# Performance work log

Hardware: AMD Instinct MI355X
Metric: run time of the kernel (lower is better)

Reference implementation:

```python
import jax, jax.numpy as jnp
import numpy as np
import math

T = 4096
HID = 2048
H = 16
D = 128
RD = 64            # rotary_dim = head_dim * partial_rotary_factor (0.5)
THETA = 10000.0
EPS = 1e-6
GROUPS = 8
LAYER_IDX = 2
N_LAYERS = 32


def build_slope_tensor(num_heads):
    def get_slopes_power_of_2(n):
        start = 2 ** (-(2 ** (-(math.log2(n) - 3))))
        ratio = start
        return [start * ratio ** i for i in range(n)]
    if math.log2(num_heads).is_integer():
        return get_slopes_power_of_2(num_heads)
    closest = 2 ** math.floor(math.log2(num_heads))
    return (get_slopes_power_of_2(closest)
            + build_slope_tensor(2 * closest)[0::2][: num_heads - closest])


def compute_slope():
    base = np.array(build_slope_tensor(H), dtype=np.float32)
    return jnp.asarray(-base * (1 - (LAYER_IDX - 1) / (N_LAYERS - 1) + 1e-5), dtype=jnp.float32)


def setup_inputs() -> dict:
    key = jax.random.key(0)
    ks = jax.random.split(key, 8)
    s = 0.02
    return {
        "positions": jnp.arange(T, dtype=jnp.int32),
        "hidden_states": jax.random.normal(ks[0], (T, HID), dtype=jnp.float32),
        "recurrent_state": jnp.zeros((1, H, D, D), dtype=jnp.float32),
        "w_qkv": jax.random.normal(ks[1], (HID, 3 * H * D), dtype=jnp.float32) * s,
        "w_g": jax.random.normal(ks[2], (HID, H * D), dtype=jnp.float32) * s,
        "w_dense": jax.random.normal(ks[3], (H * D, HID), dtype=jnp.float32) * s,
        "q_norm_w": jnp.ones((D,), dtype=jnp.float32),
        "k_norm_w": jnp.ones((D,), dtype=jnp.float32),
        "g_norm_w": jnp.ones((H * D,), dtype=jnp.float32),
    }


def _rms(x, w):
    var = jnp.mean(jnp.square(x), axis=-1, keepdims=True)
    return x * jax.lax.rsqrt(var + EPS) * w


def _rope(x, positions):
    # partial neox-style rotary on first RD dims of each head
    inv_freq = 1.0 / (THETA ** (jnp.arange(0, RD, 2, dtype=jnp.float32) / RD))
    freqs = positions.astype(jnp.float32)[:, None] * inv_freq   # [T, RD/2]
    cos = jnp.cos(freqs)[:, None, :]                            # [T, 1, RD/2]
    sin = jnp.sin(freqs)[:, None, :]
    x1 = x[..., : RD // 2]
    x2 = x[..., RD // 2 : RD]
    x_pass = x[..., RD:]
    return jnp.concatenate([x1 * cos - x2 * sin, x2 * cos + x1 * sin, x_pass], axis=-1)


def reference(positions, hidden_states, recurrent_state,
              w_qkv, w_g, w_dense, q_norm_w, k_norm_w, g_norm_w):
    t = hidden_states.shape[0]
    qkv = (hidden_states @ w_qkv).reshape(t, 3, H, D)
    q, k, v = qkv[:, 0], qkv[:, 1], qkv[:, 2]
    q = _rms(q, q_norm_w)
    k = _rms(k, k_norm_w)
    q = _rope(q, positions)
    k = _rope(k, positions)

    slope = compute_slope()                    # [H], negative
    decay = jnp.exp(slope)                     # per-head per-step decay
    scale = D ** -0.5
    q = (q * scale).astype(jnp.float32)
    k = k.astype(jnp.float32)
    v = v.astype(jnp.float32)

    def step(S, qkv_t):
        q_t, k_t, v_t = qkv_t                  # each [H, D]
        S = S * decay[:, None, None] + k_t[:, :, None] * v_t[:, None, :]
        o_t = jnp.einsum('hk,hkv->hv', q_t, S)
        return S, o_t

    S0 = recurrent_state[0].astype(jnp.float32)   # [H, K, V]
    S_final, o = jax.lax.scan(step, S0, (q, k, v))
    attn = o.reshape(t, H * D)

    gate = jax.nn.sigmoid(hidden_states @ w_g)
    # GroupRMSNorm: normalize per group of size (H*D)/GROUPS, scale by full weight
    g = attn.reshape(t, GROUPS, (H * D) // GROUPS)
    var = jnp.mean(jnp.square(g), axis=-1, keepdims=True)
    g = (g * jax.lax.rsqrt(var + EPS)).reshape(t, H * D) * g_norm_w

    out = (g * gate) @ w_dense
    return out, S_final[None]
```

## Files before the change

### kernel.cpp

```cpp
#include <hip/hip_runtime.h>
#include <hip/hip_bf16.h>

using bf16x8 = __attribute__((ext_vector_type(8))) __bf16;
using f32x4  = __attribute__((ext_vector_type(4))) float;

constexpr int T_SEQ = 4096;
constexpr int HID_C = 2048;
constexpr int NH    = 16;
constexpr int QKV_N = 6144;

__device__ __forceinline__ float head_slope(int h) {
    return -exp2f(-0.5f * (float)(h + 1)) * 0.967751935483871f;
}

__device__ __forceinline__ ushort f2bfu(float f) {
    __hip_bfloat16 h = __float2bfloat16(f);
    return *(ushort*)&h;
}
__device__ __forceinline__ float bfu2f(ushort u) {
    union { unsigned int i; float f; } x; x.i = ((unsigned int)u) << 16; return x.f;
}

__device__ __forceinline__ void async16(const ushort* g, ushort* l) {
    __builtin_amdgcn_global_load_lds((const __attribute__((address_space(1))) void*)g,
                                     (__attribute__((address_space(3))) void*)l, 16, 0, 0);
}

template<int N> __device__ __forceinline__ void waitcnt_vm() {
    if constexpr (N == 0)      asm volatile("s_waitcnt vmcnt(0)" ::: "memory");
    else if constexpr (N == 2) asm volatile("s_waitcnt vmcnt(2)" ::: "memory");
    else if constexpr (N == 4) asm volatile("s_waitcnt vmcnt(4)" ::: "memory");
    else if constexpr (N == 6) asm volatile("s_waitcnt vmcnt(6)" ::: "memory");
}

__global__ __launch_bounds__(256) void cvt_bf16(const float* __restrict__ src,
                                                ushort* __restrict__ dst, int n) {
    int i = (blockIdx.x * 256 + threadIdx.x) * 8;
    if (i >= n) return;
    float4 a = *(const float4*)(src + i);
    float4 b = *(const float4*)(src + i + 4);
    ushort4 ua = {f2bfu(a.x), f2bfu(a.y), f2bfu(a.z), f2bfu(a.w)};
    ushort4 ub = {f2bfu(b.x), f2bfu(b.y), f2bfu(b.z), f2bfu(b.w)};
    *(ushort4*)(dst + i) = ua;
    *(ushort4*)(dst + i + 4) = ub;
}

__global__ __launch_bounds__(256) void transpose_cvt(const float* __restrict__ src,
                                                     ushort* __restrict__ dst,
                                                     int R, int C) {
    __shared__ ushort tile[64][68];
    int t = threadIdx.x;
    int tr = blockIdx.y * 64, tc = blockIdx.x * 64;
    int r0 = t >> 4;
    int c4 = (t & 15) << 2;
#pragma unroll
    for (int p = 0; p < 4; ++p) {
        int row = r0 + p * 16;
        float4 v = *(const float4*)&src[(size_t)(tr + row) * C + tc + c4];
        tile[row][c4 + 0] = f2bfu(v.x);
        tile[row][c4 + 1] = f2bfu(v.y);
        tile[row][c4 + 2] = f2bfu(v.z);
        tile[row][c4 + 3] = f2bfu(v.w);
    }
    __syncthreads();
#pragma unroll
    for (int p = 0; p < 4; ++p) {
        int orow = r0 + p * 16;
        ushort4 u;
        u.x = tile[c4 + 0][orow];
        u.y = tile[c4 + 1][orow];
        u.z = tile[c4 + 2][orow];
        u.w = tile[c4 + 3][orow];
        *(ushort4*)&dst[(size_t)(tc + orow) * R + tr + c4] = u;
    }
}

template<int MI, int BN>
__device__ __forceinline__ void gemm8_core(const ushort* __restrict__ Ag,
                                           const ushort* __restrict__ Bg,
                                           int K, int bm, int bn,
                                           ushort* sh, f32x4 (&acc)[MI][4]) {
    constexpr int WM = 16 / MI;
    constexpr int WN = 8 / WM;
    constexpr int SB = BN / 128;
    constexpr int AH = (MI >= 8) ? 2 : 1;
    constexpr int MH = MI / AH;

    const int tid  = threadIdx.x;
    const int lane = tid & 63;
    const int wave = tid >> 6;
    const int lane15 = lane & 15, quad = lane >> 4;
    const int wm = wave / WN, wn = wave % WN;
    const int swz = lane15 & 7;

    ushort* const ldsA0 = sh;
    ushort* const ldsA1 = sh + 16384;
    ushort* const ldsB0 = sh + 32768;
    ushort* const ldsB1 = sh + 32768 + BN * 64;

    const int srow = lane >> 3;
    const int scol = ((lane & 7) ^ srow) << 3;
    const ushort* gA = Ag + (size_t)(bm + srow) * K + scol;
    const ushort* gB = Bg + (size_t)(bn + srow) * K + scol;
    const int ro  = wave * 16;
    const int roB = wave * 8 * SB;
    const int NT = K >> 6;

#define STAGE_A(L, k0) do { \
    _Pragma("unroll") for (int h = 0; h < 2; ++h) \
    _Pragma("unroll") for (int q = 0; q < 2; ++q) \
        async16(gA + (size_t)((h) * 128 + ro + q * 8) * K + (k0), (L) + ((h) * 128 + ro + q * 8) * 64); } while (0)
#define STAGE_B(L, k0) do { \
    _Pragma("unroll") for (int h = 0; h < 2; ++h) \
    _Pragma("unroll") for (int q = 0; q < SB; ++q) \
        async16(gB + (size_t)((h) * (BN / 2) + roB + q * 8) * K + (k0), (L) + ((h) * (BN / 2) + roB + q * 8) * 64); } while (0)

    STAGE_A(ldsA0, 0);
    STAGE_B(ldsB0, 0);
    waitcnt_vm<0>();
    asm volatile("s_barrier" ::: "memory");

    for (int t = 0; t < NT; ++t) {
        const ushort* LA = (t & 1) ? ldsA1 : ldsA0;
        const ushort* LB = (t & 1) ? ldsB1 : ldsB0;
        ushort* LAn = (t & 1) ? ldsA0 : ldsA1;
        ushort* LBn = (t & 1) ? ldsB0 : ldsB1;
        bf16x8 bfr[4][2];
#pragma unroll
        for (int j = 0; j < 4; ++j)
#pragma unroll
            for (int ks = 0; ks < 2; ++ks)
                bfr[j][ks] = *(const bf16x8*)&LB[(wn * 64 + j * 16 + lane15) * 64 + (((ks * 4 + quad) ^ swz) << 3)];
        bf16x8 af0[MH][2];
#pragma unroll
        for (int i = 0; i < MH; ++i)
#pragma unroll
            for (int ks = 0; ks < 2; ++ks)
                af0[i][ks] = *(const bf16x8*)&LA[(wm * (MI * 16) + i * 16 + lane15) * 64 + (((ks * 4 + quad) ^ swz) << 3)];
        if (t + 1 < NT) {
            STAGE_A(LAn, (t + 1) << 6);
            STAGE_B(LBn, (t + 1) << 6);
        }
        __builtin_amdgcn_s_setprio(1);
#pragma unroll
        for (int i = 0; i < MH; ++i)
#pragma unroll
            for (int j = 0; j < 4; ++j)
#pragma unroll
                for (int ks = 0; ks < 2; ++ks)
                    acc[i][j] = __builtin_amdgcn_mfma_f32_16x16x32_bf16(af0[i][ks], bfr[j][ks], acc[i][j], 0, 0, 0);
        __builtin_amdgcn_s_setprio(0);
        if constexpr (AH == 2) {
            bf16x8 af1[MH][2];
#pragma unroll
            for (int i = 0; i < MH; ++i)
#pragma unroll
                for (int ks = 0; ks < 2; ++ks)
                    af1[i][ks] = *(const bf16x8*)&LA[(wm * (MI * 16) + (MH + i) * 16 + lane15) * 64 + (((ks * 4 + quad) ^ swz) << 3)];
            __builtin_amdgcn_s_setprio(1);
#pragma unroll
            for (int i = 0; i < MH; ++i)
#pragma unroll
                for (int j = 0; j < 4; ++j)
#pragma unroll
                    for (int ks = 0; ks < 2; ++ks)
                        acc[MH + i][j] = __builtin_amdgcn_mfma_f32_16x16x32_bf16(af1[i][ks], bfr[j][ks], acc[MH + i][j], 0, 0, 0);
            __builtin_amdgcn_s_setprio(0);
        }
        waitcnt_vm<0>();
        asm volatile("s_barrier" ::: "memory");
    }
#undef STAGE_A
#undef STAGE_B
}

__global__ __launch_bounds__(512, 2) void gemm_fused(const ushort* __restrict__ A,
                                                     const ushort* __restrict__ Bcat,
                                                     ushort* __restrict__ qkv,
                                                     ushort* __restrict__ gate, int K) {
    __shared__ ushort sh[65536];
    int bid = blockIdx.x;
    int x = bid & 7, w = bid >> 3;
    int rm = x >> 2, rn = x & 3;
    int wm_i = w >> 3, wn_i = w & 7;
    int bm = (rm * 8 + wm_i) * 256;
    int bn = (rn * 8 + wn_i) * 256;
    f32x4 acc[8][4] = {};
    gemm8_core<8, 256>(A, Bcat, K, bm, bn, sh, acc);

    int lane = threadIdx.x & 63, wave = threadIdx.x >> 6;
    int lane15 = lane & 15, quad = lane >> 4;
    int wm = wave >> 2, wn = wave & 3;
    bool isg = bn >= QKV_N;
    ushort* outp = isg ? gate : qkv;
    int ncol = isg ? HID_C : QKV_N;
    int cb = (isg ? bn - QKV_N : bn) + wn * 64;
    int rb = bm + wm * 128;
#pragma unroll
    for (int i = 0; i < 8; ++i)
#pragma unroll
        for (int j = 0; j < 4; ++j) {
            int col = cb + j * 16 + lane15;
#pragma unroll
            for (int r = 0; r < 4; ++r) {
                float v = acc[i][j][r];
                if (isg) v = 1.0f / (1.0f + __expf(-v));
                outp[(size_t)(rb + i * 16 + quad * 4 + r) * ncol + col] = f2bfu(v);
            }
        }
}

__global__ __launch_bounds__(512, 2) void gemm_dense(const ushort* __restrict__ A,
                                                     const ushort* __restrict__ Bt,
                                                     float* __restrict__ Cout, int N, int K) {
    __shared__ ushort sh[49152];
    int bid = blockIdx.x;
    int x = bid & 7, w = bid >> 3;
    int rm = x >> 1, rn = x & 1;
    int wm_i = w >> 3, wn_i = w & 7;
    int bm = (rm * 4 + wm_i) * 256;
    int bn = (rn * 8 + wn_i) * 128;
    f32x4 acc[4][4] = {};
    gemm8_core<4, 128>(A, Bt, K, bm, bn, sh, acc);

    int lane = threadIdx.x & 63, wave = threadIdx.x >> 6;
    int lane15 = lane & 15, quad = lane >> 4;
    int wm = wave >> 1, wn = wave & 1;
    int cb = bn + wn * 64;
    int rb = bm + wm * 64;
#pragma unroll
    for (int i = 0; i < 4; ++i)
#pragma unroll
        for (int j = 0; j < 4; ++j) {
            int col = cb + j * 16 + lane15;
#pragma unroll
            for (int r = 0; r < 4; ++r)
                Cout[(size_t)(rb + i * 16 + quad * 4 + r) * N + col] = acc[i][j][r];
        }
}

__global__ __launch_bounds__(256) void rope_tab(const int* __restrict__ positions,
                                                float2* __restrict__ tab) {
    int i = blockIdx.x * 256 + threadIdx.x;
    int t = i >> 5, fi = i & 31;
    float inv = expf((float)fi * -0.2878231366f);
    float freq = (float)positions[t] * inv;
    float sn, cs;
    sincosf(freq, &sn, &cs);
    tab[i] = make_float2(cs, sn);
}

__global__ __launch_bounds__(256) void qk_rope_T(ushort* __restrict__ qkv,
                                                 const float2* __restrict__ tab,
                                                 const float* __restrict__ qw,
                                                 const float* __restrict__ kw,
                                                 ushort* __restrict__ kT,
                                                 ushort* __restrict__ vT) {
    __shared__ ushort tile[64][132];
    int bt = blockIdx.x;
    int kind = blockIdx.y >> 4, h = blockIdx.y & 15;
    int tid = threadIdx.x;
    int row = tid >> 2, c = tid & 3, d0 = c * 32;
    int t = bt * 64 + row;
    ushort* base = qkv + (size_t)t * QKV_N + kind * 2048 + h * 128 + d0;
    bf16x8 pk[4];
#pragma unroll
    for (int p = 0; p < 4; ++p) pk[p] = *(const bf16x8*)(base + p * 8);
    if (kind < 2) {
        float x[32];
        float ss = 0.f;
#pragma unroll
        for (int p = 0; p < 4; ++p)
#pragma unroll
            for (int i = 0; i < 8; ++i) {
                x[p * 8 + i] = (float)pk[p][i];
                ss += x[p * 8 + i] * x[p * 8 + i];
            }
        ss += __shfl_xor(ss, 1);
        ss += __shfl_xor(ss, 2);
        float rr = rsqrtf(ss * (1.0f / 128.0f) + 1e-6f);
        const float* w = (kind == 0) ? qw : kw;
#pragma unroll
        for (int i = 0; i < 32; ++i) x[i] *= rr * w[d0 + i];
#pragma unroll
        for (int i = 0; i < 32; ++i) {
            float p = __shfl_xor(x[i], 1);
            if (c < 2) {
                float2 rt = tab[t * 32 + i];
                x[i] = (c == 0) ? (x[i] * rt.x - p * rt.y) : (x[i] * rt.x + p * rt.y);
            }
        }
        float sc = (kind == 0) ? 0.08838834764831845f : 1.0f;
#pragma unroll
        for (int p = 0; p < 4; ++p)
#pragma unroll
            for (int i = 0; i < 8; ++i) pk[p][i] = (__bf16)(x[p * 8 + i] * sc);
#pragma unroll
        for (int p = 0; p < 4; ++p) *(bf16x8*)(base + p * 8) = pk[p];
    }
    if (kind >= 1) {
#pragma unroll
        for (int p = 0; p < 4; ++p) {
            ushort4* s = (ushort4*)&pk[p];
            *(ushort4*)&tile[row][d0 + p * 8]     = s[0];
            *(ushort4*)&tile[row][d0 + p * 8 + 4] = s[1];
        }
        __syncthreads();
        ushort* outT = ((kind == 1) ? kT : vT) + (size_t)(h * 128) * T_SEQ + bt * 64;
        int d = tid >> 1, half = tid & 1;
#pragma unroll
        for (int tt = 0; tt < 8; ++tt) {
            int tl = half * 32 + tt * 4;
            ushort4 u;
            u.x = tile[tl + 0][d];
            u.y = tile[tl + 1][d];
            u.z = tile[tl + 2][d];
            u.w = tile[tl + 3][d];
            *(ushort4*)&outT[(size_t)d * T_SEQ + tl] = u;
        }
    }
}

__global__ __launch_bounds__(256) void chunk_partial(const ushort* __restrict__ kT,
                                                     const ushort* __restrict__ vT,
                                                     float* __restrict__ PT) {
    int c = blockIdx.x, h = blockIdx.y;
    float slope = head_slope(h);
    float lam_inv = __expf(-slope);
    int tid = threadIdx.x, lane = tid & 63, wave = tid >> 6;
    int lane15 = lane & 15, quad = lane >> 4;
    int wv = (wave & 1) * 64, wd = (wave >> 1) * 64;
    const ushort* vbase = vT + (size_t)h * 128 * T_SEQ + c * 128;
    const ushort* kbase = kT + (size_t)h * 128 * T_SEQ + c * 128;
    f32x4 acc[4][4] = {};
#pragma unroll
    for (int j0 = 0; j0 < 128; j0 += 32) {
        float w8[8];
        w8[0] = __expf(slope * (float)(127 - (j0 + quad * 8)));
#pragma unroll
        for (int kk = 1; kk < 8; ++kk) w8[kk] = w8[kk - 1] * lam_inv;
        bf16x8 afr[4], bfr[4];
#pragma unroll
        for (int i = 0; i < 4; ++i) {
            bf16x8 v = *(const bf16x8*)&vbase[(size_t)(wv + i * 16 + lane15) * T_SEQ + j0 + quad * 8];
#pragma unroll
            for (int kk = 0; kk < 8; ++kk) afr[i][kk] = (__bf16)((float)v[kk] * w8[kk]);
        }
#pragma unroll
        for (int j = 0; j < 4; ++j)
            bfr[j] = *(const bf16x8*)&kbase[(size_t)(wd + j * 16 + lane15) * T_SEQ + j0 + quad * 8];
#pragma unroll
        for (int i = 0; i < 4; ++i)
#pragma unroll
            for (int j = 0; j < 4; ++j)
                acc[i][j] = __builtin_amdgcn_mfma_f32_16x16x32_bf16(afr[i], bfr[j], acc[i][j], 0, 0, 0);
    }
    float* out = PT + ((size_t)c * 16 + h) * 16384;
#pragma unroll
    for (int i = 0; i < 4; ++i)
#pragma unroll
        for (int j = 0; j < 4; ++j)
#pragma unroll
            for (int r = 0; r < 4; ++r)
                out[(size_t)(wv + i * 16 + quad * 4 + r) * 128 + wd + j * 16 + lane15] = acc[i][j][r];
}

__global__ __launch_bounds__(128) void scan_states(const float* __restrict__ PT,
                                                   const float* __restrict__ S0,
                                                   ushort* __restrict__ Spb,
                                                   float* __restrict__ Sfin) {
    int hv = blockIdx.x;
    int d = threadIdx.x;
    int h = hv >> 7, v = hv & 127;
    float lamC = __expf(head_slope(h) * 128.0f);
    float s = S0[(size_t)h * 16384 + d * 128 + v];
#pragma unroll
    for (int c = 0; c < 32; ++c) {
        size_t idx = ((size_t)c * 2048 + hv) * 128 + d;
        Spb[idx] = f2bfu(s);
        s = s * lamC + PT[idx];
    }
    Sfin[(size_t)h * 16384 + d * 128 + v] = s;
}

__global__ __launch_bounds__(256) void chunk_out(const ushort* __restrict__ qkv,
                                                 const ushort* __restrict__ vT,
                                                 const ushort* __restrict__ Spb,
                                                 ushort* __restrict__ o) {
    int c = blockIdx.x, h = blockIdx.y;
    float slope = head_slope(h);
    __shared__ ushort Ps[128 * 136];
    int tid = threadIdx.x, lane = tid & 63, wave = tid >> 6;
    int lane15 = lane & 15, quad = lane >> 4;
    int t0 = c * 128;
    int tt0 = wave, tt1 = 7 - wave;
    const ushort* qbase = qkv + (size_t)t0 * QKV_N + h * 128;
    const ushort* kbase = qbase + 2048;

    bf16x8 qf0[4], qf1[4];
#pragma unroll
    for (int ds = 0; ds < 4; ++ds) {
        qf0[ds] = *(const bf16x8*)&qbase[(size_t)(tt0 * 16 + lane15) * QKV_N + ds * 32 + quad * 8];
        qf1[ds] = *(const bf16x8*)&qbase[(size_t)(tt1 * 16 + lane15) * QKV_N + ds * 32 + quad * 8];
    }
    f32x4 s0a[4] = {};
    f32x4 s1a[8] = {};
#pragma unroll
    for (int st = 0; st < 8; ++st) {
        if (st <= tt1) {
            bf16x8 kf[4];
#pragma unroll
            for (int ds = 0; ds < 4; ++ds)
                kf[ds] = *(const bf16x8*)&kbase[(size_t)(st * 16 + lane15) * QKV_N + ds * 32 + quad * 8];
#pragma unroll
            for (int ds = 0; ds < 4; ++ds)
                s1a[st] = __builtin_amdgcn_mfma_f32_16x16x32_bf16(qf1[ds], kf[ds], s1a[st], 0, 0, 0);
            if (st <= tt0) {
#pragma unroll
                for (int ds = 0; ds < 4; ++ds)
                    s0a[st] = __builtin_amdgcn_mfma_f32_16x16x32_bf16(qf0[ds], kf[ds], s0a[st], 0, 0, 0);
            }
        }
    }
    int stmax0 = tt0 + ((tt0 & 1) ? 0 : 1);
    int stmax1 = tt1 + ((tt1 & 1) ? 0 : 1);
#pragma unroll
    for (int st = 0; st < 8; ++st) {
        if (st <= stmax1) {
#pragma unroll
            for (int r = 0; r < 4; ++r) {
                int t = tt1 * 16 + quad * 4 + r;
                int s = st * 16 + lane15;
                float val = 0.f;
                if (st <= tt1) val = (s <= t) ? s1a[st][r] * __expf(slope * (float)(t - s)) : 0.f;
                Ps[t * 136 + s] = f2bfu(val);
            }
        }
    }
#pragma unroll
    for (int st = 0; st < 5; ++st) {
        if (st <= stmax0) {
#pragma unroll
            for (int r = 0; r < 4; ++r) {
                int t = tt0 * 16 + quad * 4 + r;
                int s = st * 16 + lane15;
                float val = 0.f;
                if (st <= tt0) val = (s <= t) ? s0a[st][r] * __expf(slope * (float)(t - s)) : 0.f;
                Ps[t * 136 + s] = f2bfu(val);
            }
        }
    }
    __syncthreads();
    f32x4 oa0[8] = {};
    f32x4 oa1[8] = {};
    float lam0 = __expf(slope * (float)(tt0 * 16 + lane15 + 1));
    float lam1 = __expf(slope * (float)(tt1 * 16 + lane15 + 1));
    bf16x8 qs0[4], qs1[4];
#pragma unroll
    for (int ds = 0; ds < 4; ++ds)
#pragma unroll
        for (int kk = 0; kk < 8; ++kk) {
            qs0[ds][kk] = (__bf16)((float)qf0[ds][kk] * lam0);
            qs1[ds][kk] = (__bf16)((float)qf1[ds][kk] * lam1);
        }
    const ushort* spb = Spb + ((size_t)c * 2048 + h * 128) * 128;
#pragma unroll
    for (int vt = 0; vt < 8; ++vt)
#pragma unroll
        for (int ds = 0; ds < 4; ++ds) {
            bf16x8 bfrag = *(const bf16x8*)&spb[(vt * 16 + lane15) * 128 + ds * 32 + quad * 8];
            oa0[vt] = __builtin_amdgcn_mfma_f32_16x16x32_bf16(qs0[ds], bfrag, oa0[vt], 0, 0, 0);
            oa1[vt] = __builtin_amdgcn_mfma_f32_16x16x32_bf16(qs1[ds], bfrag, oa1[vt], 0, 0, 0);
        }
    const ushort* vbase = vT + (size_t)h * 128 * T_SEQ + t0;
    int ns0 = (tt0 + 2) >> 1, ns1 = (tt1 + 2) >> 1;
#pragma unroll
    for (int s32 = 0; s32 < 4; ++s32) {
        if (s32 < ns1) {
            bf16x8 af = *(const bf16x8*)&Ps[(tt1 * 16 + lane15) * 136 + s32 * 32 + quad * 8];
#pragma unroll
            for (int vt = 0; vt < 8; ++vt) {
                bf16x8 bfrag = *(const bf16x8*)&vbase[(size_t)(vt * 16 + lane15) * T_SEQ + s32 * 32 + quad * 8];
                oa1[vt] = __builtin_amdgcn_mfma_f32_16x16x32_bf16(af, bfrag, oa1[vt], 0, 0, 0);
            }
        }
    }
#pragma unroll
    for (int s32 = 0; s32 < 2; ++s32) {
        if (s32 < ns0) {
            bf16x8 af = *(const bf16x8*)&Ps[(tt0 * 16 + lane15) * 136 + s32 * 32 + quad * 8];
#pragma unroll
            for (int vt = 0; vt < 8; ++vt) {
                bf16x8 bfrag = *(const bf16x8*)&vbase[(size_t)(vt * 16 + lane15) * T_SEQ + s32 * 32 + quad * 8];
                oa0[vt] = __builtin_amdgcn_mfma_f32_16x16x32_bf16(af, bfrag, oa0[vt], 0, 0, 0);
            }
        }
    }
#pragma unroll
    for (int vt = 0; vt < 8; ++vt)
#pragma unroll
        for (int r = 0; r < 4; ++r) {
            o[(size_t)(t0 + tt0 * 16 + quad * 4 + r) * 2048 + h * 128 + vt * 16 + lane15] = f2bfu(oa0[vt][r]);
            o[(size_t)(t0 + tt1 * 16 + quad * 4 + r) * 2048 + h * 128 + vt * 16 + lane15] = f2bfu(oa1[vt][r]);
        }
}

__global__ __launch_bounds__(256) void gnorm_gate(const ushort* __restrict__ o,
                                                  const ushort* __restrict__ gate,
                                                  const float* __restrict__ gw,
                                                  ushort* __restrict__ gg) {
    int t = blockIdx.x;
    int tid = threadIdx.x;
    const ushort* op = o + (size_t)t * 2048 + tid * 8;
    bf16x8 xv = *(const bf16x8*)op;
    float x[8];
    float ss = 0.0f;
#pragma unroll
    for (int i = 0; i < 8; ++i) { x[i] = (float)xv[i]; ss += x[i] * x[i]; }
#pragma unroll
    for (int off = 16; off > 0; off >>= 1) ss += __shfl_xor(ss, off);
    float r = rsqrtf(ss * (1.0f / 256.0f) + 1e-6f);
    const ushort* gp = gate + (size_t)t * 2048;
#pragma unroll
    for (int i = 0; i < 8; ++i) {
        int j = tid * 8 + i;
        float val = x[i] * r * gw[j] * bfu2f(gp[j]);
        gg[(size_t)t * 2048 + j] = f2bfu(val);
    }
}

extern "C" void kernel_launch(void* const* d_in, const int* in_sizes, int n_in,
                              void* d_out, int out_size, void* d_ws, size_t ws_size,
                              hipStream_t stream) {
    const int* positions   = (const int*)d_in[0];
    const float* hidden    = (const float*)d_in[1];
    const float* S0        = (const float*)d_in[2];
    const float* w_qkv     = (const float*)d_in[3];
    const float* w_g       = (const float*)d_in[4];
    const float* w_dense   = (const float*)d_in[5];
    const float* qw        = (const float*)d_in[6];
    const float* kw        = (const float*)d_in[7];
    const float* gw        = (const float*)d_in[8];

    char* ws = (char*)d_ws;
    ushort* qkv     = (ushort*)ws;
    ushort* wqkv_t  = (ushort*)(ws + 50331648);
    ushort* wg_t    = (ushort*)(ws + 75497472);
    float2* ropet   = (float2*)(ws + 50331648);
    float*  PT      = (float*)(ws + 50331648);
    ushort* wd_t    = (ushort*)(ws + 83886080);
    ushort* gatebuf = (ushort*)(ws + 92274688);
    ushort* hid_b   = (ushort*)(ws + 109051904);
    ushort* Spb     = (ushort*)(ws + 109051904);
    ushort* kT      = (ushort*)(ws + 125829120);
    ushort* vT      = (ushort*)(ws + 142606336);
    ushort* gg      = (ushort*)ws;

    float* out  = (float*)d_out;
    float* Sfin = out + (size_t)T_SEQ * HID_C;
    ushort* obuf = (ushort*)d_out;

    cvt_bf16<<<T_SEQ * HID_C / (256 * 8), 256, 0, stream>>>(hidden, hid_b, T_SEQ * HID_C);
    transpose_cvt<<<dim3(QKV_N / 64, HID_C / 64), 256, 0, stream>>>(w_qkv, wqkv_t, HID_C, QKV_N);
    transpose_cvt<<<dim3(HID_C / 64, HID_C / 64), 256, 0, stream>>>(w_g, wg_t, HID_C, HID_C);
    transpose_cvt<<<dim3(HID_C / 64, HID_C / 64), 256, 0, stream>>>(w_dense, wd_t, HID_C, HID_C);

    gemm_fused<<<dim3(512), 512, 0, stream>>>(hid_b, wqkv_t, qkv, gatebuf, HID_C);

    rope_tab<<<T_SEQ * 32 / 256, 256, 0, stream>>>(positions, ropet);
    qk_rope_T<<<dim3(T_SEQ / 64, 48), 256, 0, stream>>>(qkv, ropet, qw, kw, kT, vT);

    chunk_partial<<<dim3(32, 16), 256, 0, stream>>>(kT, vT, PT);
    scan_states<<<2048, 128, 0, stream>>>(PT, S0, Spb, Sfin);
    chunk_out<<<dim3(32, 16), 256, 0, stream>>>(qkv, vT, Spb, obuf);
    gnorm_gate<<<T_SEQ, 256, 0, stream>>>(obuf, gatebuf, gw, gg);

    gemm_dense<<<dim3(256), 512, 0, stream>>>(gg, wd_t, out, HID_C, HID_C);
}
```

Measured before the change: 443.2 us.

## Merge prep kernels into one launch and retile dense GEMM to 128x128 blocks

```diff
diff --git a/kernel.cpp b/kernel.cpp
--- a/kernel.cpp
+++ b/kernel.cpp
@@ -33,10 +33,9 @@
     else if constexpr (N == 6) asm volatile("s_waitcnt vmcnt(6)" ::: "memory");
 }
 
-__global__ __launch_bounds__(256) void cvt_bf16(const float* __restrict__ src,
-                                                ushort* __restrict__ dst, int n) {
-    int i = (blockIdx.x * 256 + threadIdx.x) * 8;
-    if (i >= n) return;
+__device__ __forceinline__ void cvt_body(const float* __restrict__ src, ushort* __restrict__ dst,
+                                         int bid, int tid) {
+    int i = (bid * 256 + tid) * 8;
     float4 a = *(const float4*)(src + i);
     float4 b = *(const float4*)(src + i + 4);
     ushort4 ua = {f2bfu(a.x), f2bfu(a.y), f2bfu(a.z), f2bfu(a.w)};
@@ -45,12 +44,11 @@
     *(ushort4*)(dst + i + 4) = ub;
 }
 
-__global__ __launch_bounds__(256) void transpose_cvt(const float* __restrict__ src,
-                                                     ushort* __restrict__ dst,
-                                                     int R, int C) {
-    __shared__ ushort tile[64][68];
-    int t = threadIdx.x;
-    int tr = blockIdx.y * 64, tc = blockIdx.x * 64;
+__device__ __forceinline__ void transpose_body(const float* __restrict__ src,
+                                               ushort* __restrict__ dst,
+                                               int R, int C, int bx, int by, int t,
+                                               ushort (*tile)[68]) {
+    int tr = by * 64, tc = bx * 64;
     int r0 = t >> 4;
     int c4 = (t & 15) << 2;
 #pragma unroll
@@ -72,6 +70,40 @@
         u.z = tile[c4 + 2][orow];
         u.w = tile[c4 + 3][orow];
         *(ushort4*)&dst[(size_t)(tc + orow) * R + tr + c4] = u;
+    }
+}
+
+__global__ __launch_bounds__(256) void prep_all(const float* __restrict__ hidden,
+                                                ushort* __restrict__ hid_b,
+                                                const float* __restrict__ w_qkv,
+                                                ushort* __restrict__ wqkv_t,
+                                                const float* __restrict__ w_g,
+                                                ushort* __restrict__ wg_t,
+                                                const float* __restrict__ w_dense,
+                                                ushort* __restrict__ wd_t,
+                                                const int* __restrict__ positions,
+                                                float2* __restrict__ ropet) {
+    __shared__ ushort tile[64][68];
+    int b = blockIdx.x, t = threadIdx.x;
+    if (b < 4096) {
+        cvt_body(hidden, hid_b, b, t);
+    } else if (b < 7168) {
+        int bb = b - 4096;
+        transpose_body(w_qkv, wqkv_t, HID_C, QKV_N, bb % 96, bb / 96, t, tile);
+    } else if (b < 8192) {
+        int bb = b - 7168;
+        transpose_body(w_g, wg_t, HID_C, HID_C, bb % 32, bb / 32, t, tile);
+    } else if (b < 9216) {
+        int bb = b - 8192;
+        transpose_body(w_dense, wd_t, HID_C, HID_C, bb % 32, bb / 32, t, tile);
+    } else {
+        int i = (b - 9216) * 256 + t;
+        int tt = i >> 5, fi = i & 31;
+        float inv = expf((float)fi * -0.2878231366f);
+        float freq = (float)positions[tt] * inv;
+        float sn, cs;
+        sincosf(freq, &sn, &cs);
+        ropet[i] = make_float2(cs, sn);
     }
 }
 
@@ -172,6 +204,74 @@
     }
 #undef STAGE_A
 #undef STAGE_B
+}
+
+__device__ __forceinline__ void gemm4_core(const ushort* __restrict__ Ag,
+                                           const ushort* __restrict__ Bg,
+                                           int K, int bm, int bn,
+                                           ushort* sh, f32x4 (&acc)[4][4]) {
+    const int tid  = threadIdx.x;
+    const int lane = tid & 63;
+    const int wave = tid >> 6;
+    const int lane15 = lane & 15, quad = lane >> 4;
+    const int wm = wave >> 1, wn = wave & 1;
+    const int swz = lane15 & 7;
+
+    ushort* const ldsA0 = sh;
+    ushort* const ldsA1 = sh + 8192;
+    ushort* const ldsB0 = sh + 16384;
+    ushort* const ldsB1 = sh + 24576;
+
+    const int srow = lane >> 3;
+    const int scol = ((lane & 7) ^ srow) << 3;
+    const ushort* gA = Ag + (size_t)(bm + srow) * K + scol;
+    const ushort* gB = Bg + (size_t)(bn + srow) * K + scol;
+    const int ro = wave * 32;
+    const int NT = K >> 6;
+
+#define STG(L, g, k0) do { \
+    _Pragma("unroll") for (int q = 0; q < 4; ++q) \
+        async16((g) + (size_t)(ro + q * 8) * K + (k0), (L) + (ro + q * 8) * 64); } while (0)
+
+    STG(ldsA0, gA, 0);
+    STG(ldsB0, gB, 0);
+    waitcnt_vm<0>();
+    asm volatile("s_barrier" ::: "memory");
+
+    for (int t = 0; t < NT; ++t) {
+        const ushort* LA = (t & 1) ? ldsA1 : ldsA0;
+        const ushort* LB = (t & 1) ? ldsB1 : ldsB0;
+        ushort* LAn = (t & 1) ? ldsA0 : ldsA1;
+        ushort* LBn = (t & 1) ? ldsB0 : ldsB1;
+        bf16x8 bfr[4][2];
+#pragma unroll
+        for (int j = 0; j < 4; ++j)
+#pragma unroll
+            for (int ks = 0; ks < 2; ++ks)
+                bfr[j][ks] = *(const bf16x8*)&LB[(wn * 64 + j * 16 + lane15) * 64 + (((ks * 4 + quad) ^ swz) << 3)];
+        bf16x8 af[4][2];
+#pragma unroll
+        for (int i = 0; i < 4; ++i)
+#pragma unroll
+            for (int ks = 0; ks < 2; ++ks)
+                af[i][ks] = *(const bf16x8*)&LA[(wm * 64 + i * 16 + lane15) * 64 + (((ks * 4 + quad) ^ swz) << 3)];
+        if (t + 1 < NT) {
+            STG(LAn, gA, (t + 1) << 6);
+            STG(LBn, gB, (t + 1) << 6);
+        }
+        __builtin_amdgcn_s_setprio(1);
+#pragma unroll
+        for (int i = 0; i < 4; ++i)
+#pragma unroll
+            for (int j = 0; j < 4; ++j)
+#pragma unroll
+                for (int ks = 0; ks < 2; ++ks)
+                    acc[i][j] = __builtin_amdgcn_mfma_f32_16x16x32_bf16(af[i][ks], bfr[j][ks], acc[i][j], 0, 0, 0);
+        __builtin_amdgcn_s_setprio(0);
+        waitcnt_vm<0>();
+        asm volatile("s_barrier" ::: "memory");
+    }
+#undef STG
 }
 
 __global__ __launch_bounds__(512, 2) void gemm_fused(const ushort* __restrict__ A,
@@ -210,18 +310,18 @@
         }
 }
 
-__global__ __launch_bounds__(512, 2) void gemm_dense(const ushort* __restrict__ A,
+__global__ __launch_bounds__(256, 2) void gemm_dense(const ushort* __restrict__ A,
                                                      const ushort* __restrict__ Bt,
                                                      float* __restrict__ Cout, int N, int K) {
-    __shared__ ushort sh[49152];
+    __shared__ ushort sh[32768];
     int bid = blockIdx.x;
     int x = bid & 7, w = bid >> 3;
     int rm = x >> 1, rn = x & 1;
     int wm_i = w >> 3, wn_i = w & 7;
-    int bm = (rm * 4 + wm_i) * 256;
+    int bm = (rm * 8 + wm_i) * 128;
     int bn = (rn * 8 + wn_i) * 128;
     f32x4 acc[4][4] = {};
-    gemm8_core<4, 128>(A, Bt, K, bm, bn, sh, acc);
+    gemm4_core(A, Bt, K, bm, bn, sh, acc);
 
     int lane = threadIdx.x & 63, wave = threadIdx.x >> 6;
     int lane15 = lane & 15, quad = lane >> 4;
@@ -237,17 +337,6 @@
             for (int r = 0; r < 4; ++r)
                 Cout[(size_t)(rb + i * 16 + quad * 4 + r) * N + col] = acc[i][j][r];
         }
-}
-
-__global__ __launch_bounds__(256) void rope_tab(const int* __restrict__ positions,
-                                                float2* __restrict__ tab) {
-    int i = blockIdx.x * 256 + threadIdx.x;
-    int t = i >> 5, fi = i & 31;
-    float inv = expf((float)fi * -0.2878231366f);
-    float freq = (float)positions[t] * inv;
-    float sn, cs;
-    sincosf(freq, &sn, &cs);
-    tab[i] = make_float2(cs, sn);
 }
 
 __global__ __launch_bounds__(256) void qk_rope_T(ushort* __restrict__ qkv,
@@ -546,7 +635,7 @@
     ushort* qkv     = (ushort*)ws;
     ushort* wqkv_t  = (ushort*)(ws + 50331648);
     ushort* wg_t    = (ushort*)(ws + 75497472);
-    float2* ropet   = (float2*)(ws + 50331648);
+    float2* ropet   = (float2*)(ws + 159383552);
     float*  PT      = (float*)(ws + 50331648);
     ushort* wd_t    = (ushort*)(ws + 83886080);
     ushort* gatebuf = (ushort*)(ws + 92274688);
@@ -560,14 +649,11 @@
     float* Sfin = out + (size_t)T_SEQ * HID_C;
     ushort* obuf = (ushort*)d_out;
 
-    cvt_bf16<<<T_SEQ * HID_C / (256 * 8), 256, 0, stream>>>(hidden, hid_b, T_SEQ * HID_C);
-    transpose_cvt<<<dim3(QKV_N / 64, HID_C / 64), 256, 0, stream>>>(w_qkv, wqkv_t, HID_C, QKV_N);
-    transpose_cvt<<<dim3(HID_C / 64, HID_C / 64), 256, 0, stream>>>(w_g, wg_t, HID_C, HID_C);
-    transpose_cvt<<<dim3(HID_C / 64, HID_C / 64), 256, 0, stream>>>(w_dense, wd_t, HID_C, HID_C);
+    prep_all<<<9728, 256, 0, stream>>>(hidden, hid_b, w_qkv, wqkv_t, w_g, wg_t,
+                                       w_dense, wd_t, positions, ropet);
 
     gemm_fused<<<dim3(512), 512, 0, stream>>>(hid_b, wqkv_t, qkv, gatebuf, HID_C);
 
-    rope_tab<<<T_SEQ * 32 / 256, 256, 0, stream>>>(positions, ropet);
     qk_rope_T<<<dim3(T_SEQ / 64, 48), 256, 0, stream>>>(qkv, ropet, qw, kw, kT, vT);
 
     chunk_partial<<<dim3(32, 16), 256, 0, stream>>>(kT, vT, PT);
@@ -575,5 +661,5 @@
     chunk_out<<<dim3(32, 16), 256, 0, stream>>>(qkv, vT, Spb, obuf);
     gnorm_gate<<<T_SEQ, 256, 0, stream>>>(obuf, gatebuf, gw, gg);
 
-    gemm_dense<<<dim3(256), 512, 0, stream>>>(gg, wd_t, out, HID_C, HID_C);
-}
+    gemm_dense<<<dim3(512), 256, 0, stream>>>(gg, wd_t, out, HID_C, HID_C);
+}
```

Measured after the change: 432.2 us. 2.5% less time.
